# Kernel optimization log

Hardware: AMD Instinct MI355X
Metric: run time of the kernel (lower is better)

## Reference

```python
import jax, jax.numpy as jnp
import numpy as np

B, S, D, H = 2, 2048, 1024, 16
HD = D // H

def setup_inputs() -> dict:
    key = jax.random.key(0)
    ks = jax.random.split(key, 5)
    scale = 1.0 / np.sqrt(D)
    x = jax.random.normal(ks[0], (B, S, D), dtype=jnp.float32)
    W_qkv = jax.random.normal(ks[1], (D, 3 * D), dtype=jnp.float32) * scale
    b_qkv = jnp.zeros((3 * D,), dtype=jnp.float32)
    W_proj = jax.random.normal(ks[2], (D, D), dtype=jnp.float32) * scale
    b_proj = jnp.zeros((D,), dtype=jnp.float32)
    return {"x": x, "W_qkv": W_qkv, "b_qkv": b_qkv, "W_proj": W_proj, "b_proj": b_proj}

def reference(x, W_qkv, b_qkv, W_proj, b_proj):
    # qkv projection: [B,S,3D]
    qkv = jnp.einsum('bsd,df->bsf', x, W_qkv) + b_qkv
    q, k, v = jnp.split(qkv, 3, axis=-1)
    # reshape to heads: [B,H,S,hd]
    q = q.reshape(B, S, H, HD).transpose(0, 2, 1, 3)
    k = k.reshape(B, S, H, HD).transpose(0, 2, 1, 3)
    v = v.reshape(B, S, H, HD).transpose(0, 2, 1, 3)
    scores = jnp.einsum('bhqd,bhkd->bhqk', q, k) / jnp.sqrt(jnp.float32(HD))
    attn = jax.nn.softmax(scores, axis=-1)
    out = jnp.einsum('bhqk,bhkd->bhqd', attn, v)
    out = out.transpose(0, 2, 1, 3).reshape(B, S, D)
    return jnp.einsum('bsd,df->bsf', out, W_proj) + b_proj
```

## Files before the change

kernel.cpp:

```cpp
#include <hip/hip_runtime.h>

#define BATCH 2
#define SLEN 2048
#define DMODEL 1024
#define NHEAD 16
#define HDIM 64
#define MROWS (BATCH * SLEN)

typedef __attribute__((ext_vector_type(8))) short bf16x8;
typedef __attribute__((ext_vector_type(4))) short bf16x4;
typedef __attribute__((ext_vector_type(4))) float f32x4;
typedef __attribute__((ext_vector_type(8))) _Float16 f16x8;
typedef __attribute__((ext_vector_type(4))) _Float16 f16x4;

__device__ inline short f2bf(float x) {
    union { float f; unsigned u; } v; v.f = x;
    unsigned r = (v.u + 0x7FFFu + ((v.u >> 16) & 1u)) >> 16;
    return (short)r;
}
__device__ inline float bf2f(short h) {
    union { unsigned u; float f; } v; v.u = ((unsigned)(unsigned short)h) << 16;
    return v.f;
}
__device__ inline unsigned fbits(float x) {
    union { float f; unsigned u; } v; v.f = x; return v.u;
}
__device__ inline float hw_exp2(float x) {
    float r;
    asm("v_exp_f32 %0, %1" : "=v"(r) : "v"(x));
    return r;
}

#define NCAST (MROWS * DMODEL / 4 / 256)
#define NTW1  ((3 * DMODEL / 64) * (DMODEL / 64))
#define NTW2  ((DMODEL / 64) * (DMODEL / 64))

__global__ __launch_bounds__(256) void prep(
    const float* __restrict__ x, _Float16* __restrict__ xf,
    const float* __restrict__ Wqkv, _Float16* __restrict__ wq,
    const float* __restrict__ Wproj, _Float16* __restrict__ wp)
{
    __shared__ float T[64][68];
    int bid = blockIdx.x;
    const int tid = threadIdx.x;

    if (bid < NCAST) {
        int i = bid * 256 + tid;
        float4 f = ((const float4*)x)[i];
        f16x4 h;
        h[0] = (_Float16)f.x; h[1] = (_Float16)f.y;
        h[2] = (_Float16)f.z; h[3] = (_Float16)f.w;
        ((f16x4*)xf)[i] = h;
        return;
    }
    bid -= NCAST;

    const float* in; _Float16* outT; int N; int n0, k0;
    if (bid < NTW1) {
        in = Wqkv; outT = wq; N = 3 * DMODEL;
        n0 = (bid % 48) * 64; k0 = (bid / 48) * 64;
    } else {
        bid -= NTW1;
        in = Wproj; outT = wp; N = DMODEL;
        n0 = (bid % 16) * 64; k0 = (bid / 16) * 64;
    }
    const int K = DMODEL;

#pragma unroll
    for (int i = 0; i < 4; i++) {
        int idx = tid + i * 256;
        int r = idx >> 4, c4 = idx & 15;
        *(float4*)&T[r][c4 * 4] = *(const float4*)&in[(size_t)(k0 + r) * N + n0 + c4 * 4];
    }
    __syncthreads();
#pragma unroll
    for (int i = 0; i < 4; i++) {
        int idx = tid + i * 256;
        int n = idx >> 4, kg = idx & 15;
        f16x4 h;
#pragma unroll
        for (int j = 0; j < 4; j++)
            h[j] = (_Float16)T[kg * 4 + j][n];
        *(f16x4*)&outT[(size_t)(n0 + n) * K + k0 + kg * 4] = h;
    }
}

__global__ __launch_bounds__(256) void transpose_v(
    const short* __restrict__ qkv, short* __restrict__ vT)
{
    __shared__ short T[64 * 68];
    const int tid = threadIdx.x;
    const int bid = blockIdx.x;
    const int st = bid & 31, h = (bid >> 5) & 15, b = bid >> 9;
    const int s0 = st * 64;
    const short* src = qkv + (size_t)b * SLEN * (3 * DMODEL) + 2 * DMODEL + h * HDIM;

    const int srow = tid >> 3, sc8 = tid & 7;
#pragma unroll
    for (int it = 0; it < 2; it++) {
        int s = srow + it * 32;
        *(bf16x8*)&T[s * 68 + sc8 * 8] =
            *(const bf16x8*)&src[(size_t)(s0 + s) * (3 * DMODEL) + sc8 * 8];
    }
    __syncthreads();

    const int d = tid >> 2, sq = tid & 3;
    short* dst = vT + ((size_t)(b * NHEAD + h) * HDIM + d) * SLEN + s0 + sq * 16;
    bf16x8 o0, o1;
#pragma unroll
    for (int j = 0; j < 8; j++) {
        o0[j] = T[(sq * 16 + j) * 68 + d];
        o1[j] = T[(sq * 16 + 8 + j) * 68 + d];
    }
    *(bf16x8*)&dst[0] = o0;
    *(bf16x8*)&dst[8] = o1;
}

#define GSTR2 72

template<int OUT_BF16>
__global__ __launch_bounds__(256) void gemm_f16(
    const _Float16* __restrict__ A, const _Float16* __restrict__ Bw,
    const float* __restrict__ bias, void* __restrict__ Cout,
    int M, int N, int K)
{
    __shared__ _Float16 As[128 * GSTR2], Bs[128 * GSTR2];

    const int tid  = threadIdx.x;
    const int wave = tid >> 6, lane = tid & 63;
    const int quad = lane >> 4, lr = lane & 15;
    const int wm = (wave >> 1) * 64, wn = (wave & 1) * 64;
    const int row0 = blockIdx.y * 128, col0 = blockIdx.x * 128;

    f32x4 acc[4][4];
#pragma unroll
    for (int i = 0; i < 4; i++)
#pragma unroll
        for (int j = 0; j < 4; j++) acc[i][j] = (f32x4){0.f, 0.f, 0.f, 0.f};

    const int sr = tid >> 2, sc = tid & 3;

    const _Float16* ap0 = A  + (size_t)(row0 + sr) * K + sc * 8;
    const _Float16* ap1 = ap0 + (size_t)64 * K;
    const _Float16* bp0 = Bw + (size_t)(col0 + sr) * K + sc * 8;
    const _Float16* bp1 = bp0 + (size_t)64 * K;

    f16x8 apre[4], bpre[4];
    apre[0] = *(const f16x8*)ap0;        apre[1] = *(const f16x8*)(ap0 + 32);
    apre[2] = *(const f16x8*)ap1;        apre[3] = *(const f16x8*)(ap1 + 32);
    bpre[0] = *(const f16x8*)bp0;        bpre[1] = *(const f16x8*)(bp0 + 32);
    bpre[2] = *(const f16x8*)bp1;        bpre[3] = *(const f16x8*)(bp1 + 32);
    ap0 += 64; ap1 += 64; bp0 += 64; bp1 += 64;

    const int ls = sr * GSTR2 + sc * 8;

    for (int k0 = 0; k0 < K; k0 += 64) {
        *(f16x8*)&As[ls]                    = apre[0];
        *(f16x8*)&As[ls + 32]               = apre[1];
        *(f16x8*)&As[ls + 64 * GSTR2]       = apre[2];
        *(f16x8*)&As[ls + 64 * GSTR2 + 32]  = apre[3];
        *(f16x8*)&Bs[ls]                    = bpre[0];
        *(f16x8*)&Bs[ls + 32]               = bpre[1];
        *(f16x8*)&Bs[ls + 64 * GSTR2]       = bpre[2];
        *(f16x8*)&Bs[ls + 64 * GSTR2 + 32]  = bpre[3];

        if (k0 + 64 < K) {
            apre[0] = *(const f16x8*)ap0;        apre[1] = *(const f16x8*)(ap0 + 32);
            apre[2] = *(const f16x8*)ap1;        apre[3] = *(const f16x8*)(ap1 + 32);
            bpre[0] = *(const f16x8*)bp0;        bpre[1] = *(const f16x8*)(bp0 + 32);
            bpre[2] = *(const f16x8*)bp1;        bpre[3] = *(const f16x8*)(bp1 + 32);
            ap0 += 64; ap1 += 64; bp0 += 64; bp1 += 64;
        }

        __syncthreads();

#pragma unroll
        for (int kk = 0; kk < 2; kk++) {
            f16x8 af[4];
#pragma unroll
            for (int mt = 0; mt < 4; mt++)
                af[mt] = *(const f16x8*)&As[(wm + mt * 16 + lr) * GSTR2 + kk * 32 + quad * 8];
#pragma unroll
            for (int nt = 0; nt < 4; nt++) {
                f16x8 b = *(const f16x8*)&Bs[(wn + nt * 16 + lr) * GSTR2 + kk * 32 + quad * 8];
#pragma unroll
                for (int mt = 0; mt < 4; mt++)
                    acc[mt][nt] = __builtin_amdgcn_mfma_f32_16x16x32_f16(af[mt], b, acc[mt][nt], 0, 0, 0);
            }
        }

        __syncthreads();
    }

#pragma unroll
    for (int mt = 0; mt < 4; mt++) {
#pragma unroll
        for (int nt = 0; nt < 4; nt++) {
            int col = col0 + wn + nt * 16 + lr;
            float bv = bias[col];
#pragma unroll
            for (int r = 0; r < 4; r++) {
                int row = row0 + wm + mt * 16 + quad * 4 + r;
                float v = acc[mt][nt][r] + bv;
                if (OUT_BF16)
                    ((short*)Cout)[(size_t)row * N + col] = f2bf(v);
                else
                    ((float*)Cout)[(size_t)row * N + col] = v;
            }
        }
    }
}

#define ASTR 72
#define NT   (SLEN / 64)
#define RSTR 20
#define QK_SCALE_LOG2E 0.1803368801111244f

__global__ __launch_bounds__(256) void attn_mfma(
    const short* __restrict__ qkv, const short* __restrict__ vT,
    _Float16* __restrict__ attn)
{
    __shared__ __align__(16) char smem[2 * 64 * ASTR * 2 * 2];
    short* KsBuf = (short*)smem;
    short* VtBuf = KsBuf + 2 * 64 * ASTR;

    const int tid  = threadIdx.x;
    const int lane = tid & 63;
    const int wave = tid >> 6;
    const int quad = lane >> 4;
    const int lr   = lane & 15;
    const int qhalf  = wave >> 1;
    const int cthalf = wave & 1;

    const int bid = blockIdx.x;
    const int qt = bid & 31;
    const int h  = (bid >> 5) & 15;
    const int b  = bid >> 9;
    const int q0 = qt * 64;

    const short* qbase = qkv + (size_t)b * SLEN * (3 * DMODEL) + h * HDIM;
    const short* kbase = qbase + DMODEL;
    const short* vtbase = vT + (size_t)(b * NHEAD + h) * HDIM * SLEN;

    bf16x8 qf[2][2];
#pragma unroll
    for (int qs = 0; qs < 2; qs++)
#pragma unroll
        for (int ds2 = 0; ds2 < 2; ds2++) {
            bf16x8 q = *(const bf16x8*)&qbase[(size_t)(q0 + qhalf * 32 + qs * 16 + lr) * (3 * DMODEL) + ds2 * 32 + quad * 8];
#pragma unroll
            for (int j = 0; j < 8; j++)
                q[j] = f2bf(bf2f(q[j]) * QK_SCALE_LOG2E);
            qf[qs][ds2] = q;
        }

    bf16x4 ones;
#pragma unroll
    for (int j = 0; j < 4; j++) ones[j] = (short)0x3F80;

    f32x4 oacc[2][4];
#pragma unroll
    for (int qs = 0; qs < 2; qs++)
#pragma unroll
        for (int t = 0; t < 4; t++) oacc[qs][t] = (f32x4){0.f, 0.f, 0.f, 0.f};
    f32x4 sacc[2] = {{0.f, 0.f, 0.f, 0.f}, {0.f, 0.f, 0.f, 0.f}};

    const int srow = tid >> 3, sc8 = tid & 7;

    const short* kp0 = kbase + (size_t)srow * (3 * DMODEL) + sc8 * 8;
    const short* kp1 = kp0 + 32 * (3 * DMODEL);
    const short* vp0 = vtbase + (size_t)srow * SLEN + sc8 * 8;
    const short* vp1 = vp0 + 32 * SLEN;

    bf16x8 kpre[2], vpre[2];
    kpre[0] = *(const bf16x8*)kp0; kpre[1] = *(const bf16x8*)kp1;
    vpre[0] = *(const bf16x8*)vp0; vpre[1] = *(const bf16x8*)vp1;
    kp0 += 64 * (3 * DMODEL); kp1 += 64 * (3 * DMODEL);
    vp0 += 64; vp1 += 64;

    for (int kt = 0; kt < NT; kt++) {
        const int cur = kt & 1;
        short* ks = KsBuf + cur * 64 * ASTR;
        short* vt = VtBuf + cur * 64 * ASTR;

        *(bf16x8*)&ks[srow * ASTR + sc8 * 8] = kpre[0];
        *(bf16x8*)&ks[(srow + 32) * ASTR + sc8 * 8] = kpre[1];
        *(bf16x8*)&vt[srow * ASTR + sc8 * 8] = vpre[0];
        *(bf16x8*)&vt[(srow + 32) * ASTR + sc8 * 8] = vpre[1];

        if (kt + 1 < NT) {
            kpre[0] = *(const bf16x8*)kp0; kpre[1] = *(const bf16x8*)kp1;
            vpre[0] = *(const bf16x8*)vp0; vpre[1] = *(const bf16x8*)vp1;
            kp0 += 64 * (3 * DMODEL); kp1 += 64 * (3 * DMODEL);
            vp0 += 64; vp1 += 64;
        }

        __syncthreads();

#pragma unroll
        for (int ct2 = 0; ct2 < 2; ct2++) {
            const int ct = cthalf * 2 + ct2;
            bf16x8 kf0 = *(const bf16x8*)&ks[(ct * 16 + lr) * ASTR + quad * 8];
            bf16x8 kf1 = *(const bf16x8*)&ks[(ct * 16 + lr) * ASTR + 32 + quad * 8];
            bf16x4 vf0 = *(const bf16x4*)&vt[(0 * 16 + lr) * ASTR + ct * 16 + quad * 4];
            bf16x4 vf1 = *(const bf16x4*)&vt[(1 * 16 + lr) * ASTR + ct * 16 + quad * 4];
            bf16x4 vf2 = *(const bf16x4*)&vt[(2 * 16 + lr) * ASTR + ct * 16 + quad * 4];
            bf16x4 vf3 = *(const bf16x4*)&vt[(3 * 16 + lr) * ASTR + ct * 16 + quad * 4];

#pragma unroll
            for (int qs = 0; qs < 2; qs++) {
                f32x4 st = {0.f, 0.f, 0.f, 0.f};
                st = __builtin_amdgcn_mfma_f32_16x16x32_bf16(kf0, qf[qs][0], st, 0, 0, 0);
                st = __builtin_amdgcn_mfma_f32_16x16x32_bf16(kf1, qf[qs][1], st, 0, 0, 0);

                float p0[4];
#pragma unroll
                for (int r = 0; r < 4; r++) p0[r] = hw_exp2(st[r]);
                union { uint2 u; bf16x4 v; } pk0;
                pk0.u.x = __builtin_amdgcn_perm(fbits(p0[1]), fbits(p0[0]), 0x07060302u);
                pk0.u.y = __builtin_amdgcn_perm(fbits(p0[3]), fbits(p0[2]), 0x07060302u);
                bf16x4 pf0 = pk0.v;

                sacc[qs] = __builtin_amdgcn_mfma_f32_16x16x16bf16_1k(ones, pf0, sacc[qs], 0, 0, 0);
                oacc[qs][0] = __builtin_amdgcn_mfma_f32_16x16x16bf16_1k(vf0, pf0, oacc[qs][0], 0, 0, 0);
                oacc[qs][1] = __builtin_amdgcn_mfma_f32_16x16x16bf16_1k(vf1, pf0, oacc[qs][1], 0, 0, 0);
                oacc[qs][2] = __builtin_amdgcn_mfma_f32_16x16x16bf16_1k(vf2, pf0, oacc[qs][2], 0, 0, 0);
                oacc[qs][3] = __builtin_amdgcn_mfma_f32_16x16x16bf16_1k(vf3, pf0, oacc[qs][3], 0, 0, 0);
            }
        }
    }

    __syncthreads();
    float* Lf = (float*)smem;
    float* myrow = Lf + (wave * 64 + lane) * RSTR;

    if (cthalf == 1) {
        *(f32x4*)&myrow[0]  = oacc[0][0];
        *(f32x4*)&myrow[4]  = oacc[0][1];
        *(f32x4*)&myrow[8]  = oacc[0][2];
        *(f32x4*)&myrow[12] = oacc[0][3];
        myrow[16] = sacc[0][0];
    }
    __syncthreads();
    if (cthalf == 0) {
        const float* pr = Lf + ((wave ^ 1) * 64 + lane) * RSTR;
        f32x4 o0 = oacc[0][0] + *(const f32x4*)&pr[0];
        f32x4 o1 = oacc[0][1] + *(const f32x4*)&pr[4];
        f32x4 o2 = oacc[0][2] + *(const f32x4*)&pr[8];
        f32x4 o3 = oacc[0][3] + *(const f32x4*)&pr[12];
        const float inv = 1.0f / (sacc[0][0] + pr[16]);
        const int row = b * SLEN + q0 + qhalf * 32 + lr;
        f16x4 h4;
#pragma unroll
        for (int r = 0; r < 4; r++) h4[r] = (_Float16)(o0[r] * inv);
        *(f16x4*)&attn[(size_t)row * DMODEL + h * HDIM + 0 * 16 + quad * 4] = h4;
#pragma unroll
        for (int r = 0; r < 4; r++) h4[r] = (_Float16)(o1[r] * inv);
        *(f16x4*)&attn[(size_t)row * DMODEL + h * HDIM + 1 * 16 + quad * 4] = h4;
#pragma unroll
        for (int r = 0; r < 4; r++) h4[r] = (_Float16)(o2[r] * inv);
        *(f16x4*)&attn[(size_t)row * DMODEL + h * HDIM + 2 * 16 + quad * 4] = h4;
#pragma unroll
        for (int r = 0; r < 4; r++) h4[r] = (_Float16)(o3[r] * inv);
        *(f16x4*)&attn[(size_t)row * DMODEL + h * HDIM + 3 * 16 + quad * 4] = h4;
        *(f32x4*)&myrow[0]  = oacc[1][0];
        *(f32x4*)&myrow[4]  = oacc[1][1];
        *(f32x4*)&myrow[8]  = oacc[1][2];
        *(f32x4*)&myrow[12] = oacc[1][3];
        myrow[16] = sacc[1][0];
    }
    __syncthreads();
    if (cthalf == 1) {
        const float* pr = Lf + ((wave ^ 1) * 64 + lane) * RSTR;
        f32x4 o0 = oacc[1][0] + *(const f32x4*)&pr[0];
        f32x4 o1 = oacc[1][1] + *(const f32x4*)&pr[4];
        f32x4 o2 = oacc[1][2] + *(const f32x4*)&pr[8];
        f32x4 o3 = oacc[1][3] + *(const f32x4*)&pr[12];
        const float inv = 1.0f / (sacc[1][0] + pr[16]);
        const int row = b * SLEN + q0 + qhalf * 32 + 16 + lr;
        f16x4 h4;
#pragma unroll
        for (int r = 0; r < 4; r++) h4[r] = (_Float16)(o0[r] * inv);
        *(f16x4*)&attn[(size_t)row * DMODEL + h * HDIM + 0 * 16 + quad * 4] = h4;
#pragma unroll
        for (int r = 0; r < 4; r++) h4[r] = (_Float16)(o1[r] * inv);
        *(f16x4*)&attn[(size_t)row * DMODEL + h * HDIM + 1 * 16 + quad * 4] = h4;
#pragma unroll
        for (int r = 0; r < 4; r++) h4[r] = (_Float16)(o2[r] * inv);
        *(f16x4*)&attn[(size_t)row * DMODEL + h * HDIM + 2 * 16 + quad * 4] = h4;
#pragma unroll
        for (int r = 0; r < 4; r++) h4[r] = (_Float16)(o3[r] * inv);
        *(f16x4*)&attn[(size_t)row * DMODEL + h * HDIM + 3 * 16 + quad * 4] = h4;
    }
}

extern "C" void kernel_launch(void* const* d_in, const int* in_sizes, int n_in,
                              void* d_out, int out_size, void* d_ws, size_t ws_size,
                              hipStream_t stream) {
    (void)in_sizes; (void)n_in; (void)out_size; (void)ws_size;
    const float* x     = (const float*)d_in[0];
    const float* Wqkv  = (const float*)d_in[1];
    const float* bqkv  = (const float*)d_in[2];
    const float* Wproj = (const float*)d_in[3];
    const float* bproj = (const float*)d_in[4];
    float* out = (float*)d_out;

    short* qkv = (short*)d_ws;
    _Float16* xf = (_Float16*)(qkv + (size_t)MROWS * 3 * DMODEL);
    _Float16* wq = xf + (size_t)MROWS * DMODEL;
    _Float16* wp = wq + (size_t)3 * DMODEL * DMODEL;
    short* vT = (short*)(wp + (size_t)DMODEL * DMODEL);
    _Float16* attnb = (_Float16*)(vT + (size_t)MROWS * DMODEL);

    prep<<<dim3(NCAST + NTW1 + NTW2), 256, 0, stream>>>(x, xf, Wqkv, wq, Wproj, wp);

    gemm_f16<1><<<dim3(3 * DMODEL / 128, MROWS / 128), 256, 0, stream>>>(
        xf, wq, bqkv, (void*)qkv, MROWS, 3 * DMODEL, DMODEL);

    transpose_v<<<dim3(BATCH * NHEAD * (SLEN / 64)), 256, 0, stream>>>(qkv, vT);

    attn_mfma<<<dim3(BATCH * NHEAD * (SLEN / 64)), 256, 0, stream>>>(qkv, vT, attnb);

    gemm_f16<0><<<dim3(DMODEL / 128, MROWS / 128), 256, 0, stream>>>(
        attnb, wp, bproj, (void*)out, MROWS, DMODEL, DMODEL);
}
```

Before: 196.3 us.

## Load GEMM tiles directly into LDS with XOR-swizzled layout

Replaces the register-prefetch plus LDS store path in the f16 GEMM with global_load_lds direct-to-LDS transfers. An XOR swizzle on 16-byte chunks replaces the padded stride so that fragment reads avoid bank conflicts. This cuts VGPR staging and LDS write instructions, but it drops the register double-buffering, so global loads are no longer overlapped with MFMA compute within a block.

```diff
diff --git a/kernel.cpp b/kernel.cpp
--- a/kernel.cpp
+++ b/kernel.cpp
@@ -116,7 +116,7 @@
     *(bf16x8*)&dst[8] = o1;
 }
 
-#define GSTR2 72
+#define BK 64
 
 template<int OUT_BF16>
 __global__ __launch_bounds__(256) void gemm_f16(
@@ -124,7 +124,7 @@
     const float* __restrict__ bias, void* __restrict__ Cout,
     int M, int N, int K)
 {
-    __shared__ _Float16 As[128 * GSTR2], Bs[128 * GSTR2];
+    __shared__ _Float16 As[128 * BK], Bs[128 * BK];
 
     const int tid  = threadIdx.x;
     const int wave = tid >> 6, lane = tid & 63;
@@ -138,58 +138,44 @@
 #pragma unroll
         for (int j = 0; j < 4; j++) acc[i][j] = (f32x4){0.f, 0.f, 0.f, 0.f};
 
-    const int sr = tid >> 2, sc = tid & 3;
-
-    const _Float16* ap0 = A  + (size_t)(row0 + sr) * K + sc * 8;
-    const _Float16* ap1 = ap0 + (size_t)64 * K;
-    const _Float16* bp0 = Bw + (size_t)(col0 + sr) * K + sc * 8;
-    const _Float16* bp1 = bp0 + (size_t)64 * K;
-
-    f16x8 apre[4], bpre[4];
-    apre[0] = *(const f16x8*)ap0;        apre[1] = *(const f16x8*)(ap0 + 32);
-    apre[2] = *(const f16x8*)ap1;        apre[3] = *(const f16x8*)(ap1 + 32);
-    bpre[0] = *(const f16x8*)bp0;        bpre[1] = *(const f16x8*)(bp0 + 32);
-    bpre[2] = *(const f16x8*)bp1;        bpre[3] = *(const f16x8*)(bp1 + 32);
-    ap0 += 64; ap1 += 64; bp0 += 64; bp1 += 64;
-
-    const int ls = sr * GSTR2 + sc * 8;
-
-    for (int k0 = 0; k0 < K; k0 += 64) {
-        *(f16x8*)&As[ls]                    = apre[0];
-        *(f16x8*)&As[ls + 32]               = apre[1];
-        *(f16x8*)&As[ls + 64 * GSTR2]       = apre[2];
-        *(f16x8*)&As[ls + 64 * GSTR2 + 32]  = apre[3];
-        *(f16x8*)&Bs[ls]                    = bpre[0];
-        *(f16x8*)&Bs[ls + 32]               = bpre[1];
-        *(f16x8*)&Bs[ls + 64 * GSTR2]       = bpre[2];
-        *(f16x8*)&Bs[ls + 64 * GSTR2 + 32]  = bpre[3];
-
-        if (k0 + 64 < K) {
-            apre[0] = *(const f16x8*)ap0;        apre[1] = *(const f16x8*)(ap0 + 32);
-            apre[2] = *(const f16x8*)ap1;        apre[3] = *(const f16x8*)(ap1 + 32);
-            bpre[0] = *(const f16x8*)bp0;        bpre[1] = *(const f16x8*)(bp0 + 32);
-            bpre[2] = *(const f16x8*)bp1;        bpre[3] = *(const f16x8*)(bp1 + 32);
-            ap0 += 64; ap1 += 64; bp0 += 64; bp1 += 64;
-        }
-
+    const int srl = lane >> 3;
+    const int scl = lane & 7;
+    const int swz = scl ^ srl;
+
+    for (int k0 = 0; k0 < K; k0 += BK) {
         __syncthreads();
+#pragma unroll
+        for (int i = 0; i < 4; i++) {
+            const int rbase = i * 32 + wave * 8;
+            const int r = rbase + srl;
+            __builtin_amdgcn_global_load_lds(
+                (const __attribute__((address_space(1))) unsigned int*)
+                    &A[(size_t)(row0 + r) * K + k0 + swz * 8],
+                (__attribute__((address_space(3))) unsigned int*)&As[rbase * BK],
+                16, 0, 0);
+            __builtin_amdgcn_global_load_lds(
+                (const __attribute__((address_space(1))) unsigned int*)
+                    &Bw[(size_t)(col0 + r) * K + k0 + swz * 8],
+                (__attribute__((address_space(3))) unsigned int*)&Bs[rbase * BK],
+                16, 0, 0);
+        }
+        __syncthreads();
 
 #pragma unroll
         for (int kk = 0; kk < 2; kk++) {
+            const int cb = ((kk * 4 + quad) ^ (lr & 7)) * 8;
             f16x8 af[4];
 #pragma unroll
             for (int mt = 0; mt < 4; mt++)
-                af[mt] = *(const f16x8*)&As[(wm + mt * 16 + lr) * GSTR2 + kk * 32 + quad * 8];
+                af[mt] = *(const f16x8*)&As[(wm + mt * 16 + lr) * BK + cb];
 #pragma unroll
             for (int nt = 0; nt < 4; nt++) {
-                f16x8 b = *(const f16x8*)&Bs[(wn + nt * 16 + lr) * GSTR2 + kk * 32 + quad * 8];
+                f16x8 b = *(const f16x8*)&Bs[(wn + nt * 16 + lr) * BK + cb];
 #pragma unroll
                 for (int mt = 0; mt < 4; mt++)
                     acc[mt][nt] = __builtin_amdgcn_mfma_f32_16x16x32_f16(af[mt], b, acc[mt][nt], 0, 0, 0);
             }
         }
-
-        __syncthreads();
     }
 
 #pragma unroll
```

Measured after the change: 210.4 us. +7.2%, slower.
